# Performance work log

Hardware: AMD Instinct MI355X
Metric: run time of the kernel (lower is better)

The kernel has to match this reference:

```python
import jax, jax.numpy as jnp
import numpy as np

B, C_IN, C_TMP, C_OUT, N = 4, 256, 256, 256, 4096


def setup_inputs() -> dict:
    key = jax.random.key(0)
    k1, k2, k3, k4 = jax.random.split(key, 4)
    scale = 1.0 / np.sqrt(C_IN)
    return {
        "fea": jax.random.normal(k1, (B, C_IN, N), dtype=jnp.float32),
        "Wq": jax.random.normal(k2, (C_TMP, C_IN), dtype=jnp.float32) * scale,
        "Wk": jax.random.normal(k3, (C_TMP, C_IN), dtype=jnp.float32) * scale,
        "Wv": jax.random.normal(k4, (C_OUT, C_IN), dtype=jnp.float32) * scale,
    }


def reference(fea, Wq, Wk, Wv):
    # 1x1 Conv1d == per-point channel matmul
    Q = jnp.einsum("ti,bin->btn", Wq, fea)   # (B, temp, N)
    K = jnp.einsum("ti,bin->btn", Wk, fea)   # (B, temp, N)
    V = jnp.einsum("oi,bin->bon", Wv, fea)   # (B, out, N)
    # S[b, i, j] = sum_t K[b, t, i] * Q[b, t, j]; note: no 1/sqrt(d) scaling
    S = jnp.einsum("bti,btj->bij", K, Q)     # (B, N, N)
    S = jax.nn.softmax(S, axis=1)            # softmax over key axis (dim=1)
    new_fea = jnp.einsum("bok,bkn->bon", V, S)  # (B, out, N)
    # merge == 'concat'
    out = jnp.concatenate([new_fea, fea], axis=1)  # (B, out+in, N)
    return jax.nn.relu(out)
```

## Files before the change

### kernel.cpp

```cpp
#include <hip/hip_runtime.h>

#define NB 4
#define C  256
#define NN 4096

typedef _Float16 half8   __attribute__((ext_vector_type(8)));
typedef _Float16 h2      __attribute__((ext_vector_type(2)));
typedef float    f32x4   __attribute__((ext_vector_type(4)));
typedef float    f32x16  __attribute__((ext_vector_type(16)));

static __device__ __forceinline__ f32x4 mfma16(half8 a, half8 b, f32x4 c) {
    return __builtin_amdgcn_mfma_f32_16x16x32_f16(a, b, c, 0, 0, 0);
}
static __device__ __forceinline__ f32x16 mfma32(half8 a, half8 b, f32x16 c) {
    return __builtin_amdgcn_mfma_f32_32x32x16_f16(a, b, c, 0, 0, 0);
}
static __device__ __forceinline__ void gld16(const void* g, void* l) {
    __builtin_amdgcn_global_load_lds(
        (const __attribute__((address_space(1))) unsigned int*)g,
        (__attribute__((address_space(3))) unsigned int*)l, 16, 0, 0);
}
static __device__ __forceinline__ unsigned cvtpk_u(float a, float b) {
    auto r = __builtin_amdgcn_cvt_pkrtz(a, b);
    return *reinterpret_cast<unsigned*>(&r);
}

__global__ __launch_bounds__(256) void proj_kernel(
    const float* __restrict__ fea, const float* __restrict__ Wq,
    const float* __restrict__ Wk, const float* __restrict__ Wv,
    _Float16* __restrict__ Qt, _Float16* __restrict__ Kt,
    _Float16* __restrict__ Vp, float* __restrict__ out)
{
    const int lin = blockIdx.x + gridDim.x * blockIdx.y;
    const int xcd = lin & 7;
    const int b   = xcd >> 1;
    const int nt  = ((lin >> 3) << 1) | (xcd & 1);
    const int n0  = nt * 32;

    __shared__ __align__(16) _Float16 fh[32][264];

    const int tid = threadIdx.x;
    {
        const int nl = tid & 31, rr = tid >> 5;
        const float* feab = fea + (size_t)b * C * NN + n0 + nl;
        float* outb = out + (size_t)b * 2 * C * NN + (size_t)C * NN + n0 + nl;
#pragma unroll
        for (int p = 0; p < 32; ++p) {
            const int i = p * 8 + rr;
            const float v = feab[(size_t)i * NN];
            outb[(size_t)i * NN] = fmaxf(v, 0.f);
            fh[nl][i] = (_Float16)v;
        }
    }
    __syncthreads();

    const int w = tid >> 6, lane = tid & 63, lr = lane & 15, lg = lane >> 4;

    const float* const Ws[2] = {Wq, Wk};
    _Float16* const   Od[2] = {Qt + (size_t)b * NN * C, Kt + (size_t)b * NN * C};
#pragma unroll 1
    for (int qk = 0; qk < 2; ++qk) {
        const float* __restrict__ W = Ws[qk];
        f32x4 acc[2][4];
#pragma unroll
        for (int mi = 0; mi < 2; ++mi)
#pragma unroll
            for (int ni = 0; ni < 4; ++ni) acc[mi][ni] = (f32x4){0.f, 0.f, 0.f, 0.f};

#pragma unroll 1
        for (int kt = 0; kt < 8; ++kt) {
            half8 ah[2];
#pragma unroll
            for (int mi = 0; mi < 2; ++mi)
                ah[mi] = *(const half8*)&fh[mi * 16 + lr][kt * 32 + lg * 8];
            half8 bh[4];
#pragma unroll
            for (int ni = 0; ni < 4; ++ni) {
                const float* src = W + (size_t)(w * 64 + ni * 16 + lr) * C + kt * 32 + lg * 8;
                const float4 x0 = *(const float4*)src;
                const float4 x1 = *(const float4*)(src + 4);
                bh[ni][0] = (_Float16)x0.x; bh[ni][1] = (_Float16)x0.y;
                bh[ni][2] = (_Float16)x0.z; bh[ni][3] = (_Float16)x0.w;
                bh[ni][4] = (_Float16)x1.x; bh[ni][5] = (_Float16)x1.y;
                bh[ni][6] = (_Float16)x1.z; bh[ni][7] = (_Float16)x1.w;
            }
#pragma unroll
            for (int mi = 0; mi < 2; ++mi)
#pragma unroll
                for (int ni = 0; ni < 4; ++ni)
                    acc[mi][ni] = mfma16(ah[mi], bh[ni], acc[mi][ni]);
        }
        _Float16* dst = Od[qk];
#pragma unroll
        for (int mi = 0; mi < 2; ++mi)
#pragma unroll
            for (int ni = 0; ni < 4; ++ni)
#pragma unroll
                for (int r = 0; r < 4; ++r)
                    dst[(size_t)(n0 + mi * 16 + lg * 4 + r) * C + (w * 64 + ni * 16 + lr)] =
                        (_Float16)acc[mi][ni][r];
    }

    {
        f32x4 acc[4][2];
#pragma unroll
        for (int mi = 0; mi < 4; ++mi)
#pragma unroll
            for (int ni = 0; ni < 2; ++ni) acc[mi][ni] = (f32x4){0.f, 0.f, 0.f, 0.f};

#pragma unroll 1
        for (int kt = 0; kt < 8; ++kt) {
            half8 ah[4];
#pragma unroll
            for (int mi = 0; mi < 4; ++mi) {
                const float* src = Wv + (size_t)(w * 64 + mi * 16 + lr) * C + kt * 32 + lg * 8;
                const float4 x0 = *(const float4*)src;
                const float4 x1 = *(const float4*)(src + 4);
                ah[mi][0] = (_Float16)x0.x; ah[mi][1] = (_Float16)x0.y;
                ah[mi][2] = (_Float16)x0.z; ah[mi][3] = (_Float16)x0.w;
                ah[mi][4] = (_Float16)x1.x; ah[mi][5] = (_Float16)x1.y;
                ah[mi][6] = (_Float16)x1.z; ah[mi][7] = (_Float16)x1.w;
            }
            half8 bh[2];
#pragma unroll
            for (int ni = 0; ni < 2; ++ni)
                bh[ni] = *(const half8*)&fh[ni * 16 + lr][kt * 32 + lg * 8];
#pragma unroll
            for (int mi = 0; mi < 4; ++mi)
#pragma unroll
                for (int ni = 0; ni < 2; ++ni)
                    acc[mi][ni] = mfma16(ah[mi], bh[ni], acc[mi][ni]);
        }
        _Float16* vb = Vp + (size_t)b * C * NN;
#pragma unroll
        for (int mi = 0; mi < 4; ++mi)
#pragma unroll
            for (int ni = 0; ni < 2; ++ni)
#pragma unroll
                for (int r = 0; r < 4; ++r)
                    vb[(size_t)(w * 64 + mi * 16 + lg * 4 + r) * NN + n0 + ni * 16 + lr] =
                        (_Float16)acc[mi][ni][r];
    }
}

template<int KS>
__global__ __launch_bounds__(256, 2) void attn4(
    const _Float16* __restrict__ Qt, const _Float16* __restrict__ Kt,
    const _Float16* __restrict__ Vp, _Float16* __restrict__ Opart,
    float* __restrict__ ml, float* __restrict__ out)
{
    extern __shared__ char smem[];

    const int lin = blockIdx.x;
    const int xcd = lin & 7, slot = lin >> 3;
    int b, ks, jt;
    if constexpr (KS == 4) {
        const int combo = xcd * 2 + (slot >> 5);
        b = combo >> 2; ks = combo & 3; jt = slot & 31;
    } else {
        b = xcd >> 1; ks = 0; jt = ((slot & 15) << 1) | (xcd & 1);
    }

    const int tid = threadIdx.x;
    const int wv = tid >> 6, lane = tid & 63;
    const int l31 = lane & 31, hi = lane >> 5;
    const int j0 = jt * 128 + wv * 32;
    const int iBase = ks * (NN / KS);
    const int T = (NN / KS) / 32;

    const _Float16* Qb = Qt + (size_t)b * NN * C;
    const char* Kg = (const char*)(Kt + (size_t)b * NN * C);
    const char* Vg = (const char*)(Vp + (size_t)b * C * NN);

    half8 q[16];
#pragma unroll
    for (int kk = 0; kk < 16; ++kk)
        q[kk] = *(const half8*)(Qb + (size_t)(j0 + l31) * C + kk * 16 + hi * 8);

    f32x16 O[8];
#pragma unroll
    for (int ob = 0; ob < 8; ++ob) O[ob] = (f32x16)(0.f);
    float m = -1e30f, ll = 0.f;

#define STAGE(nb, t_) do {                                                     \
    const int i0_ = iBase + (t_) * 32;                                         \
    char* dK_ = smem + ((nb) ? 16384 : 0);                                     \
    char* dV_ = smem + 32768 + ((nb) ? 16384 : 0);                             \
    _Pragma("unroll")                                                          \
    for (int r_ = 0; r_ < 4; ++r_) {                                           \
        const int p_ = r_ * 4096 + tid * 16;                                   \
        const int row_ = p_ >> 9, c1_ = (p_ >> 4) & 31;                        \
        gld16(Kg + (size_t)(i0_ + row_) * 512 + ((c1_ ^ row_) << 4), dK_ + p_);\
    }                                                                          \
    _Pragma("unroll")                                                          \
    for (int r_ = 0; r_ < 4; ++r_) {                                           \
        const int p_ = r_ * 4096 + tid * 16;                                   \
        const int mac_ = p_ >> 9, c1_ = (p_ >> 4) & 31;                        \
        const int o_ = mac_ * 8 + (c1_ >> 2);                                  \
        gld16(Vg + (size_t)o_ * (NN * 2) + (size_t)i0_ * 2 +                   \
                  (((c1_ & 3) ^ (mac_ & 3)) << 4), dV_ + p_);                  \
    }                                                                          \
} while (0)

    STAGE(0, 0);

#pragma unroll 1
    for (int t = 0; t < T; ++t) {
        __syncthreads();
        if (t + 1 < T) STAGE((t + 1) & 1, t + 1);

        const char* kb = smem + ((t & 1) ? 16384 : 0);
        const char* vb = smem + 32768 + ((t & 1) ? 16384 : 0);

        f32x16 s = (f32x16)(0.f);
#pragma unroll
        for (int kk = 0; kk < 16; ++kk) {
            const half8 a = *(const half8*)(kb + l31 * 512 + (((kk * 2 + hi) ^ l31) << 4));
            s = mfma32(a, q[kk], s);
        }

        float tmax = s[0];
#pragma unroll
        for (int r = 1; r < 16; ++r) tmax = fmaxf(tmax, s[r]);
        tmax = fmaxf(tmax, __shfl_xor(tmax, 32, 64));
        if (__any(tmax > m + 8.0f)) {
            const float mn = fmaxf(m, tmax);
            const float sc = __expf(m - mn);
            m = mn;
            ll *= sc;
#pragma unroll
            for (int ob = 0; ob < 8; ++ob) O[ob] *= sc;
        }

        float lsum = 0.f;
#pragma unroll
        for (int r = 0; r < 16; ++r) { s[r] = __expf(s[r] - m); lsum += s[r]; }
        ll += lsum;

        unsigned P0 = cvtpk_u(s[0], s[1]),   P1 = cvtpk_u(s[2], s[3]);
        unsigned P2 = cvtpk_u(s[4], s[5]),   P3 = cvtpk_u(s[6], s[7]);
        unsigned P4 = cvtpk_u(s[8], s[9]),   P5 = cvtpk_u(s[10], s[11]);
        unsigned P6 = cvtpk_u(s[12], s[13]), P7 = cvtpk_u(s[14], s[15]);
        const unsigned x0 = __shfl_xor((int)P0, 32, 64), x1 = __shfl_xor((int)P1, 32, 64);
        const unsigned x2 = __shfl_xor((int)P2, 32, 64), x3 = __shfl_xor((int)P3, 32, 64);
        const unsigned x4 = __shfl_xor((int)P4, 32, 64), x5 = __shfl_xor((int)P5, 32, 64);
        const unsigned x6 = __shfl_xor((int)P6, 32, 64), x7 = __shfl_xor((int)P7, 32, 64);
        int4 fw0, fw1;
        fw0.x = hi ? x2 : P0;  fw0.y = hi ? x3 : P1;
        fw0.z = hi ? P2 : x0;  fw0.w = hi ? P3 : x1;
        fw1.x = hi ? x6 : P4;  fw1.y = hi ? x7 : P5;
        fw1.z = hi ? P6 : x4;  fw1.w = hi ? P7 : x5;
        const half8 f0 = *reinterpret_cast<half8*>(&fw0);
        const half8 f1 = *reinterpret_cast<half8*>(&fw1);

#pragma unroll
        for (int ob = 0; ob < 8; ++ob) {
            const int o = ob * 32 + l31;
            const int mac = o >> 3;
            const char* vrow = vb + mac * 512;
            const int cb = (l31 & 7) * 4;
            const int xr = l31 >> 3;
            const half8 v0 = *(const half8*)(vrow + ((cb + ((0 + hi) ^ xr)) << 4));
            const half8 v1 = *(const half8*)(vrow + ((cb + ((2 + hi) ^ xr)) << 4));
            O[ob] = mfma32(v0, f0, O[ob]);
            O[ob] = mfma32(v1, f1, O[ob]);
        }
    }

    const float lt = ll + __shfl_xor(ll, 32, 64);
    const float il = 1.f / lt;

    if constexpr (KS == 4) {
        if (hi == 0) {
            float* mlb = ml + (size_t)(b * KS + ks) * 2 * NN;
            mlb[j0 + l31] = m;
            mlb[NN + j0 + l31] = lt;
        }
        _Float16* op = Opart + (size_t)(b * KS + ks) * C * NN;
#pragma unroll
        for (int ob = 0; ob < 8; ++ob)
#pragma unroll
            for (int w = 0; w < 8; ++w) {
                const int o = ob * 32 + ((2 * w) & 3) + 8 * (w >> 1) + 4 * hi;
                op[(size_t)o * NN + j0 + l31]       = (_Float16)(O[ob][2 * w] * il);
                op[(size_t)(o + 1) * NN + j0 + l31] = (_Float16)(O[ob][2 * w + 1] * il);
            }
    } else {
        float* obp = out + (size_t)b * 2 * C * NN;
#pragma unroll
        for (int ob = 0; ob < 8; ++ob)
#pragma unroll
            for (int w = 0; w < 8; ++w) {
                const int o = ob * 32 + ((2 * w) & 3) + 8 * (w >> 1) + 4 * hi;
                obp[(size_t)o * NN + j0 + l31]       = fmaxf(O[ob][2 * w] * il, 0.f);
                obp[(size_t)(o + 1) * NN + j0 + l31] = fmaxf(O[ob][2 * w + 1] * il, 0.f);
            }
    }
#undef STAGE
}

template<int KS>
__global__ __launch_bounds__(256) void combine_kernel(
    const _Float16* __restrict__ Opart, const float* __restrict__ ml,
    float* __restrict__ out)
{
    const int b = blockIdx.x >> 6, cc = blockIdx.x & 63;
    const int tid = threadIdx.x;
    const int col = cc * 64 + (tid & 63);
    const int op0 = tid >> 6;
    float mv[KS], wgt[KS];
    float M = -1e30f;
#pragma unroll
    for (int s = 0; s < KS; ++s) {
        mv[s] = ml[(size_t)(b * KS + s) * 2 * NN + col];
        M = fmaxf(M, mv[s]);
    }
    float L = 0.f;
#pragma unroll
    for (int s = 0; s < KS; ++s) {
        const float lv = ml[((size_t)(b * KS + s) * 2 + 1) * NN + col];
        wgt[s] = __expf(mv[s] - M) * lv; L += wgt[s];
    }
    const float invL = 1.f / L;
#pragma unroll
    for (int s = 0; s < KS; ++s) wgt[s] *= invL;
    float* ob = out + (size_t)b * 2 * C * NN + col;
    for (int oit = 0; oit < 64; ++oit) {
        const int o = oit * 4 + op0;
        float acc = 0.f;
#pragma unroll
        for (int s = 0; s < KS; ++s)
            acc += wgt[s] * (float)Opart[((size_t)(b * KS + s) * C + o) * NN + col];
        ob[(size_t)o * NN] = fmaxf(acc, 0.f);
    }
}

extern "C" void kernel_launch(void* const* d_in, const int* in_sizes, int n_in,
                              void* d_out, int out_size, void* d_ws, size_t ws_size,
                              hipStream_t stream) {
    const float* fea = (const float*)d_in[0];
    const float* Wq  = (const float*)d_in[1];
    const float* Wk  = (const float*)d_in[2];
    const float* Wv  = (const float*)d_in[3];
    float* out = (float*)d_out;

    _Float16* Qt = (_Float16*)d_ws;
    _Float16* Kt = Qt + (size_t)NB * NN * C;
    _Float16* Vp = Kt + (size_t)NB * NN * C;
    char* extra = (char*)(Vp + (size_t)NB * NN * C);
    const size_t base = (size_t)3 * NB * NN * C * sizeof(_Float16);

    proj_kernel<<<dim3(128, 4), 256, 0, stream>>>(fea, Wq, Wk, Wv, Qt, Kt, Vp, out);

    const int SMEM = 65536;
    const size_t need4 = base + (size_t)4 * NB * C * NN * 2 + (size_t)4 * NB * 2 * NN * 4;

    if (ws_size >= need4) {
        _Float16* Op = (_Float16*)extra;
        float* mlp = (float*)(extra + (size_t)4 * NB * C * NN * 2);
        (void)hipFuncSetAttribute(reinterpret_cast<const void*>(&attn4<4>),
                                  hipFuncAttributeMaxDynamicSharedMemorySize, SMEM);
        attn4<4><<<512, 256, SMEM, stream>>>(Qt, Kt, Vp, Op, mlp, out);
        combine_kernel<4><<<NB * 64, 256, 0, stream>>>(Op, mlp, out);
    } else {
        (void)hipFuncSetAttribute(reinterpret_cast<const void*>(&attn4<1>),
                                  hipFuncAttributeMaxDynamicSharedMemorySize, SMEM);
        attn4<1><<<128, 256, SMEM, stream>>>(Qt, Kt, Vp, nullptr, nullptr, out);
    }
}
```

Baseline: 158.2 us.

## Pre-convert weights to fp16, split QK MFMA chain, add wave priority hints

A new small kernel converts Wq, Wk and Wv to fp16 once per call, so the projection kernel loads half8 weights directly instead of converting fp32 on every load. In the attention kernel the 16-step score MFMA chain is split into two independent accumulators that are summed afterwards, shortening the dependency chain. s_setprio hints are placed around the MFMA sections to favour waves issuing matrix ops. This adds one extra kernel launch and workspace for the fp16 weights.

```diff
diff --git a/kernel.cpp b/kernel.cpp
--- a/kernel.cpp
+++ b/kernel.cpp
@@ -5,7 +5,6 @@
 #define NN 4096
 
 typedef _Float16 half8   __attribute__((ext_vector_type(8)));
-typedef _Float16 h2      __attribute__((ext_vector_type(2)));
 typedef float    f32x4   __attribute__((ext_vector_type(4)));
 typedef float    f32x16  __attribute__((ext_vector_type(16)));
 
@@ -25,9 +24,23 @@
     return *reinterpret_cast<unsigned*>(&r);
 }
 
+__global__ __launch_bounds__(256) void wcvt_kernel(
+    const float* __restrict__ Wq, const float* __restrict__ Wk,
+    const float* __restrict__ Wv, _Float16* __restrict__ Wh)
+{
+    const int which = blockIdx.y;
+    const float* src = which == 0 ? Wq : (which == 1 ? Wk : Wv);
+    _Float16* dst = Wh + (size_t)which * (C * C);
+    const int idx = blockIdx.x * 1024 + threadIdx.x * 4;
+    const float4 v = *(const float4*)(src + idx);
+    uint2 pk;
+    pk.x = cvtpk_u(v.x, v.y);
+    pk.y = cvtpk_u(v.z, v.w);
+    *(uint2*)(dst + idx) = pk;
+}
+
 __global__ __launch_bounds__(256) void proj_kernel(
-    const float* __restrict__ fea, const float* __restrict__ Wq,
-    const float* __restrict__ Wk, const float* __restrict__ Wv,
+    const float* __restrict__ fea, const _Float16* __restrict__ Wh,
     _Float16* __restrict__ Qt, _Float16* __restrict__ Kt,
     _Float16* __restrict__ Vp, float* __restrict__ out)
 {
@@ -56,11 +69,11 @@
 
     const int w = tid >> 6, lane = tid & 63, lr = lane & 15, lg = lane >> 4;
 
-    const float* const Ws[2] = {Wq, Wk};
-    _Float16* const   Od[2] = {Qt + (size_t)b * NN * C, Kt + (size_t)b * NN * C};
+    const _Float16* const Ws[2] = {Wh, Wh + C * C};
+    _Float16* const       Od[2] = {Qt + (size_t)b * NN * C, Kt + (size_t)b * NN * C};
 #pragma unroll 1
     for (int qk = 0; qk < 2; ++qk) {
-        const float* __restrict__ W = Ws[qk];
+        const _Float16* __restrict__ W = Ws[qk];
         f32x4 acc[2][4];
 #pragma unroll
         for (int mi = 0; mi < 2; ++mi)
@@ -75,15 +88,8 @@
                 ah[mi] = *(const half8*)&fh[mi * 16 + lr][kt * 32 + lg * 8];
             half8 bh[4];
 #pragma unroll
-            for (int ni = 0; ni < 4; ++ni) {
-                const float* src = W + (size_t)(w * 64 + ni * 16 + lr) * C + kt * 32 + lg * 8;
-                const float4 x0 = *(const float4*)src;
-                const float4 x1 = *(const float4*)(src + 4);
-                bh[ni][0] = (_Float16)x0.x; bh[ni][1] = (_Float16)x0.y;
-                bh[ni][2] = (_Float16)x0.z; bh[ni][3] = (_Float16)x0.w;
-                bh[ni][4] = (_Float16)x1.x; bh[ni][5] = (_Float16)x1.y;
-                bh[ni][6] = (_Float16)x1.z; bh[ni][7] = (_Float16)x1.w;
-            }
+            for (int ni = 0; ni < 4; ++ni)
+                bh[ni] = *(const half8*)(W + (size_t)(w * 64 + ni * 16 + lr) * C + kt * 32 + lg * 8);
 #pragma unroll
             for (int mi = 0; mi < 2; ++mi)
 #pragma unroll
@@ -102,6 +108,7 @@
     }
 
     {
+        const _Float16* __restrict__ Wv16 = Wh + 2 * C * C;
         f32x4 acc[4][2];
 #pragma unroll
         for (int mi = 0; mi < 4; ++mi)
@@ -112,15 +119,8 @@
         for (int kt = 0; kt < 8; ++kt) {
             half8 ah[4];
 #pragma unroll
-            for (int mi = 0; mi < 4; ++mi) {
-                const float* src = Wv + (size_t)(w * 64 + mi * 16 + lr) * C + kt * 32 + lg * 8;
-                const float4 x0 = *(const float4*)src;
-                const float4 x1 = *(const float4*)(src + 4);
-                ah[mi][0] = (_Float16)x0.x; ah[mi][1] = (_Float16)x0.y;
-                ah[mi][2] = (_Float16)x0.z; ah[mi][3] = (_Float16)x0.w;
-                ah[mi][4] = (_Float16)x1.x; ah[mi][5] = (_Float16)x1.y;
-                ah[mi][6] = (_Float16)x1.z; ah[mi][7] = (_Float16)x1.w;
-            }
+            for (int mi = 0; mi < 4; ++mi)
+                ah[mi] = *(const half8*)(Wv16 + (size_t)(w * 64 + mi * 16 + lr) * C + kt * 32 + lg * 8);
             half8 bh[2];
 #pragma unroll
             for (int ni = 0; ni < 2; ++ni)
@@ -144,7 +144,7 @@
 }
 
 template<int KS>
-__global__ __launch_bounds__(256, 2) void attn4(
+__global__ __launch_bounds__(256, 2) void attn6(
     const _Float16* __restrict__ Qt, const _Float16* __restrict__ Kt,
     const _Float16* __restrict__ Vp, _Float16* __restrict__ Opart,
     float* __restrict__ ml, float* __restrict__ out)
@@ -212,12 +212,17 @@
         const char* kb = smem + ((t & 1) ? 16384 : 0);
         const char* vb = smem + 32768 + ((t & 1) ? 16384 : 0);
 
-        f32x16 s = (f32x16)(0.f);
-#pragma unroll
-        for (int kk = 0; kk < 16; ++kk) {
-            const half8 a = *(const half8*)(kb + l31 * 512 + (((kk * 2 + hi) ^ l31) << 4));
-            s = mfma32(a, q[kk], s);
-        }
+        f32x16 sA = (f32x16)(0.f), sB = (f32x16)(0.f);
+        __builtin_amdgcn_s_setprio(1);
+#pragma unroll
+        for (int kk = 0; kk < 8; ++kk) {
+            const half8 a0 = *(const half8*)(kb + l31 * 512 + (((kk * 2 + hi) ^ l31) << 4));
+            const half8 a1 = *(const half8*)(kb + l31 * 512 + ((((kk + 8) * 2 + hi) ^ l31) << 4));
+            sA = mfma32(a0, q[kk], sA);
+            sB = mfma32(a1, q[kk + 8], sB);
+        }
+        __builtin_amdgcn_s_setprio(0);
+        f32x16 s = sA + sB;
 
         float tmax = s[0];
 #pragma unroll
@@ -253,6 +258,7 @@
         const half8 f0 = *reinterpret_cast<half8*>(&fw0);
         const half8 f1 = *reinterpret_cast<half8*>(&fw1);
 
+        __builtin_amdgcn_s_setprio(1);
 #pragma unroll
         for (int ob = 0; ob < 8; ++ob) {
             const int o = ob * 32 + l31;
@@ -265,6 +271,7 @@
             O[ob] = mfma32(v0, f0, O[ob]);
             O[ob] = mfma32(v1, f1, O[ob]);
         }
+        __builtin_amdgcn_s_setprio(0);
     }
 
     const float lt = ll + __shfl_xor(ll, 32, 64);
@@ -347,24 +354,26 @@
     _Float16* Qt = (_Float16*)d_ws;
     _Float16* Kt = Qt + (size_t)NB * NN * C;
     _Float16* Vp = Kt + (size_t)NB * NN * C;
-    char* extra = (char*)(Vp + (size_t)NB * NN * C);
-    const size_t base = (size_t)3 * NB * NN * C * sizeof(_Float16);
-
-    proj_kernel<<<dim3(128, 4), 256, 0, stream>>>(fea, Wq, Wk, Wv, Qt, Kt, Vp, out);
+    _Float16* Wh = Vp + (size_t)NB * NN * C;
+    char* extra = (char*)(Wh + (size_t)3 * C * C);
+    const size_t baseW = ((size_t)3 * NB * NN * C + (size_t)3 * C * C) * sizeof(_Float16);
+
+    wcvt_kernel<<<dim3(64, 3), 256, 0, stream>>>(Wq, Wk, Wv, Wh);
+    proj_kernel<<<dim3(128, 4), 256, 0, stream>>>(fea, Wh, Qt, Kt, Vp, out);
 
     const int SMEM = 65536;
-    const size_t need4 = base + (size_t)4 * NB * C * NN * 2 + (size_t)4 * NB * 2 * NN * 4;
+    const size_t need4 = baseW + (size_t)4 * NB * C * NN * 2 + (size_t)4 * NB * 2 * NN * 4;
 
     if (ws_size >= need4) {
         _Float16* Op = (_Float16*)extra;
         float* mlp = (float*)(extra + (size_t)4 * NB * C * NN * 2);
-        (void)hipFuncSetAttribute(reinterpret_cast<const void*>(&attn4<4>),
+        (void)hipFuncSetAttribute(reinterpret_cast<const void*>(&attn6<4>),
                                   hipFuncAttributeMaxDynamicSharedMemorySize, SMEM);
-        attn4<4><<<512, 256, SMEM, stream>>>(Qt, Kt, Vp, Op, mlp, out);
+        attn6<4><<<512, 256, SMEM, stream>>>(Qt, Kt, Vp, Op, mlp, out);
         combine_kernel<4><<<NB * 64, 256, 0, stream>>>(Op, mlp, out);
     } else {
-        (void)hipFuncSetAttribute(reinterpret_cast<const void*>(&attn4<1>),
+        (void)hipFuncSetAttribute(reinterpret_cast<const void*>(&attn6<1>),
                                   hipFuncAttributeMaxDynamicSharedMemorySize, SMEM);
-        attn4<1><<<128, 256, SMEM, stream>>>(Qt, Kt, Vp, nullptr, nullptr, out);
-    }
-}
+        attn6<1><<<128, 256, SMEM, stream>>>(Qt, Kt, Vp, nullptr, nullptr, out);
+    }
+}
```

New measurement: 156.9 us. Within noise of the previous version (-0.8%).
